# Kernel optimization log

Hardware: AMD Instinct MI355X
Metric: run time of the kernel (lower is better)

Reference implementation:

```python
import jax, jax.numpy as jnp
import numpy as np

TEMPERATURE = 0.01  # clamped min is 0.01, so constant temp stays 0.01
MASK_VAL = -10000.0


def setup_inputs() -> dict:
    key = jax.random.key(0)
    k1, k2 = jax.random.split(key)
    B, C, D = 512, 16, 128
    ts_features = jax.random.normal(k1, (B, C, D), dtype=jnp.float32)
    note_features = jax.random.normal(k2, (B, C, D), dtype=jnp.float32)
    return {"ts_features": ts_features, "note_features": note_features}


def reference(ts_features, note_features):
    B, C, D = ts_features.shape
    N = B * C
    ts = ts_features.reshape(N, D)
    nt = note_features.reshape(N, D)

    # sim[i, j] = <ts_i, nt_j>
    sim = jnp.einsum('id,jd->ij', ts, nt)

    # block-diagonal mask: within each CxC block, off-diagonal -> -10000, diagonal kept
    idx = jnp.arange(N)
    blk = idx // C
    same_block = blk[:, None] == blk[None, :]
    is_diag = idx[:, None] == idx[None, :]
    sim_new = jnp.where(same_block & ~is_diag, jnp.asarray(MASK_VAL, sim.dtype), sim)

    logits = sim_new / TEMPERATURE
    # cross entropy with labels = arange(N), both directions
    lsm_r = jax.nn.log_softmax(logits, axis=-1)
    lsm_c = jax.nn.log_softmax(logits.T, axis=-1)
    diag_ids = (idx, idx)
    ce_r = -jnp.mean(lsm_r[diag_ids])
    ce_c = -jnp.mean(lsm_c[diag_ids])
    total_loss = (ce_r + ce_c) / 2

    # nan/inf -> 0 as in the original
    total_loss = jnp.where(jnp.isnan(total_loss) | jnp.isinf(total_loss),
                           jnp.asarray(0.0, total_loss.dtype), total_loss)
    return total_loss
```

## Files before the change

kernel.cpp:

```cpp
#include <hip/hip_runtime.h>
#include <stdint.h>

#define NROWS 8192
#define DDIM  128
#define PPART 8
#define BROWS 256
#define NITER 16
#define LOG2E_X100 144.26950408889634f
#define LN2F       0.6931471805599453f

typedef __bf16 bf16x8 __attribute__((ext_vector_type(8)));
typedef float  f32x4  __attribute__((ext_vector_type(4)));
typedef unsigned short u16x8 __attribute__((ext_vector_type(8)));


__device__ __forceinline__ unsigned short f2bf_rne(float f) {
    union { float f; uint32_t u; } v; v.f = f;
    uint32_t r = (v.u + 0x7FFFu + ((v.u >> 16) & 1u)) >> 16;
    return (unsigned short)r;
}

__device__ __forceinline__ void async16(const unsigned short* g, unsigned char* l) {
    __builtin_amdgcn_global_load_lds(
        (const __attribute__((address_space(1))) unsigned int*)g,
        (__attribute__((address_space(3))) unsigned int*)l, 16, 0, 0);
}

__global__ void convert_kernel(const float* __restrict__ ts, const float* __restrict__ nt,
                               unsigned short* __restrict__ ts_bf,
                               unsigned short* __restrict__ nt_bf,
                               float* __restrict__ acc, int* __restrict__ ticket) {
    const int nchunk = (NROWS * DDIM) / 8;
    int tid = blockIdx.x * blockDim.x + threadIdx.x;
    bool isNT = tid >= nchunk;
    int i = isNT ? (tid - nchunk) : tid;
    const float4* src = (const float4*)(isNT ? nt : ts) + i * 2;
    float4 v0 = src[0], v1 = src[1];
    float sc = isNT ? 1.0f : LOG2E_X100;
    u16x8 o;
    o[0] = f2bf_rne(v0.x * sc); o[1] = f2bf_rne(v0.y * sc);
    o[2] = f2bf_rne(v0.z * sc); o[3] = f2bf_rne(v0.w * sc);
    o[4] = f2bf_rne(v1.x * sc); o[5] = f2bf_rne(v1.y * sc);
    o[6] = f2bf_rne(v1.z * sc); o[7] = f2bf_rne(v1.w * sc);
    int row = i >> 4, chunk = i & 15;
    int g = row >> 4, c = row & 15;
    int kc = chunk >> 2, quad = chunk & 3;
    int off16 = (g * 4 + kc) * 64 + quad * 16 + c;
    ((u16x8*)(isNT ? nt_bf : ts_bf))[off16] = o;
    if (tid == 0) { *acc = 0.0f; *ticket = 0; }
}

__device__ __forceinline__ void dma_stage(const unsigned short* g, unsigned char* l,
                                          int lane, int wv) {
#pragma unroll
    for (int k = 0; k < 2; ++k) {
        int u = wv * 2 + k;
        async16(g + u * 512 + lane * 8, l + u * 1024);
    }
}

__global__ __launch_bounds__(512, 4) void rowstats_kernel(
        const unsigned short* __restrict__ ts_bf,
        const unsigned short* __restrict__ nt_bf,
        float* __restrict__ pm, float* __restrict__ ps, float* __restrict__ pd) {
    __shared__ unsigned char smem[2 * 16384];

    const int lane = threadIdx.x & 63;
    const int wv   = threadIdx.x >> 6;
    const int c    = lane & 15;
    const int quad = lane >> 4;
    const int bx   = blockIdx.x;
    const int part = blockIdx.y;
    const int dir  = blockIdx.z;
    const int rows0 = bx * BROWS + wv * 32;

    const unsigned short* A = dir ? nt_bf : ts_bf;
    const unsigned short* B = dir ? ts_bf : nt_bf;

    const int G0 = bx * 16 + wv * 2;
    bf16x8 a[2][4];
#pragma unroll
    for (int s = 0; s < 2; ++s)
#pragma unroll
        for (int kc = 0; kc < 4; ++kc)
            a[s][kc] = *(const bf16x8*)(A + ((G0 + s) * 4 + kc) * 512 + lane * 8);

    float m[2][4], ss[2][4], dg[2][4];
#pragma unroll
    for (int s = 0; s < 2; ++s)
#pragma unroll
        for (int r = 0; r < 4; ++r) { m[s][r] = -INFINITY; ss[s][r] = 0.0f; dg[s][r] = 0.0f; }

    const bool havePart = (part == (bx >> 2));
    const int  t_d = (bx & 3) * 4 + (wv >> 1);
    const int  l0  = (wv & 1) * 2;

    const unsigned short* bwalk = B + part * 64 * 2048;

    dma_stage(bwalk, smem, lane, wv);
    __syncthreads();

    for (int t = 0; t < NITER; ++t) {
        if (t + 1 < NITER)
            dma_stage(bwalk + (t + 1) * 8192, smem + ((t + 1) & 1) * 16384, lane, wv);

        const unsigned char* buf = smem + (t & 1) * 16384 + lane * 16;

        f32x4 av[4][2];
#pragma unroll
        for (int l = 0; l < 4; ++l)
#pragma unroll
            for (int s = 0; s < 2; ++s) av[l][s] = (f32x4){0.f, 0.f, 0.f, 0.f};

#pragma unroll
        for (int kc = 0; kc < 4; ++kc) {
            bf16x8 b0 = *(const bf16x8*)(buf + kc * 1024);
            bf16x8 b1 = *(const bf16x8*)(buf + kc * 1024 + 4096);
            bf16x8 b2 = *(const bf16x8*)(buf + kc * 1024 + 8192);
            bf16x8 b3 = *(const bf16x8*)(buf + kc * 1024 + 12288);
            av[0][0] = __builtin_amdgcn_mfma_f32_16x16x32_bf16(a[0][kc], b0, av[0][0], 0, 0, 0);
            av[0][1] = __builtin_amdgcn_mfma_f32_16x16x32_bf16(a[1][kc], b0, av[0][1], 0, 0, 0);
            av[1][0] = __builtin_amdgcn_mfma_f32_16x16x32_bf16(a[0][kc], b1, av[1][0], 0, 0, 0);
            av[1][1] = __builtin_amdgcn_mfma_f32_16x16x32_bf16(a[1][kc], b1, av[1][1], 0, 0, 0);
            av[2][0] = __builtin_amdgcn_mfma_f32_16x16x32_bf16(a[0][kc], b2, av[2][0], 0, 0, 0);
            av[2][1] = __builtin_amdgcn_mfma_f32_16x16x32_bf16(a[1][kc], b2, av[2][1], 0, 0, 0);
            av[3][0] = __builtin_amdgcn_mfma_f32_16x16x32_bf16(a[0][kc], b3, av[3][0], 0, 0, 0);
            av[3][1] = __builtin_amdgcn_mfma_f32_16x16x32_bf16(a[1][kc], b3, av[3][1], 0, 0, 0);
        }

        const bool pd_ = havePart && (t == t_d);
#pragma unroll
        for (int s = 0; s < 2; ++s) {
#pragma unroll
            for (int r = 0; r < 4; ++r) {
                float x0 = av[0][s][r], x1 = av[1][s][r];
                float x2 = av[2][s][r], x3 = av[3][s][r];
                if (pd_) {
                    const int dslot = l0 + s;
                    bool onDiag = (c == quad * 4 + r);
                    float xv = dslot == 0 ? x0 : dslot == 1 ? x1 : dslot == 2 ? x2 : x3;
                    if (onDiag) dg[s][r] += xv;
                    float rep = onDiag ? xv : -1.0e30f;
                    if (dslot == 0) x0 = rep; else if (dslot == 1) x1 = rep;
                    else if (dslot == 2) x2 = rep; else x3 = rep;
                }
                float mn = fmaxf(fmaxf(fmaxf(x0, x1), fmaxf(x2, x3)), m[s][r]);
                float e  = __builtin_amdgcn_exp2f(m[s][r] - mn);
                float es = (__builtin_amdgcn_exp2f(x0 - mn) + __builtin_amdgcn_exp2f(x1 - mn))
                         + (__builtin_amdgcn_exp2f(x2 - mn) + __builtin_amdgcn_exp2f(x3 - mn));
                ss[s][r] = fmaf(ss[s][r], e, es);
                m[s][r] = mn;
            }
        }
        __syncthreads();
    }

#pragma unroll
    for (int s = 0; s < 2; ++s) {
#pragma unroll
        for (int r = 0; r < 4; ++r) {
            float mm = m[s][r];
#pragma unroll
            for (int off = 1; off < 16; off <<= 1)
                mm = fmaxf(mm, __shfl_xor(mm, off, 64));
            float sv = ss[s][r] * __builtin_amdgcn_exp2f(m[s][r] - mm);
            float dd = dg[s][r];
#pragma unroll
            for (int off = 1; off < 16; off <<= 1) {
                sv += __shfl_xor(sv, off, 64);
                dd += __shfl_xor(dd, off, 64);
            }
            if (c == 0) {
                int row = rows0 + s * 16 + quad * 4 + r;
                int idx = (dir * NROWS + row) * PPART + part;
                pm[idx] = mm; ps[idx] = sv; pd[idx] = dd;
            }
        }
    }
}

__global__ void merge_kernel(const float* __restrict__ pm, const float* __restrict__ ps,
                             const float* __restrict__ pd, float* __restrict__ acc,
                             int* __restrict__ ticket, float* __restrict__ out) {
    int tid = blockIdx.x * blockDim.x + threadIdx.x;
    const float* pmr = pm + tid * PPART;
    const float* psr = ps + tid * PPART;
    const float* pdr = pd + tid * PPART;
    float mt = -INFINITY;
#pragma unroll
    for (int p = 0; p < PPART; ++p) mt = fmaxf(mt, pmr[p]);
    float st = 0.0f, dt = 0.0f;
#pragma unroll
    for (int p = 0; p < PPART; ++p) {
        st += psr[p] * __builtin_amdgcn_exp2f(pmr[p] - mt);
        dt += pdr[p];
    }
    float lsm = dt - mt - __builtin_amdgcn_logf(st);

    float v = lsm;
#pragma unroll
    for (int off = 32; off; off >>= 1) v += __shfl_down(v, off, 64);
    __shared__ float wsum[4];
    if ((threadIdx.x & 63) == 0) wsum[threadIdx.x >> 6] = v;
    __syncthreads();
    if (threadIdx.x == 0) {
        atomicAdd(acc, wsum[0] + wsum[1] + wsum[2] + wsum[3]);
        __threadfence();
        int old = atomicAdd(ticket, 1);
        if (old == (int)gridDim.x - 1) {
            __threadfence();
            float tot = atomicAdd(acc, 0.0f);
            float t = -(tot * LN2F) / (2.0f * NROWS);
            if (!isfinite(t)) t = 0.0f;
            out[0] = t;
        }
    }
}

extern "C" void kernel_launch(void* const* d_in, const int* in_sizes, int n_in,
                              void* d_out, int out_size, void* d_ws, size_t ws_size,
                              hipStream_t stream) {
    const float* ts = (const float*)d_in[0];
    const float* nt = (const float*)d_in[1];
    float* out = (float*)d_out;

    unsigned short* ts_bf = (unsigned short*)d_ws;
    unsigned short* nt_bf = ts_bf + NROWS * DDIM;
    float* pm = (float*)(nt_bf + NROWS * DDIM);
    float* ps = pm + 2 * NROWS * PPART;
    float* pd = ps + 2 * NROWS * PPART;
    float* acc = pd + 2 * NROWS * PPART;
    int* ticket = (int*)(acc + 1);

    convert_kernel<<<1024, 256, 0, stream>>>(ts, nt, ts_bf, nt_bf, acc, ticket);
    rowstats_kernel<<<dim3(NROWS / BROWS, PPART, 2), 512, 0, stream>>>(ts_bf, nt_bf, pm, ps, pd);
    merge_kernel<<<(2 * NROWS) / 256, 256, 0, stream>>>(pm, ps, pd, acc, ticket, out);
}
```

Before: 107.4 us.

## Compute row and column softmax stats from one shared similarity tile

Each 256x256 block of the similarity matrix is now computed once, and both its row-wise and column-wise log-sum-exp partials are reduced from it. Previously the matrix was computed twice, once per direction. This halves the MFMA work. In exchange the kernel does extra exp2 and cross-lane shuffles for the column reduction, adds LDS traffic, and the merge kernel reads 32 partials per row for each of rows and columns.

```diff
diff --git a/kernel.cpp b/kernel.cpp
--- a/kernel.cpp
+++ b/kernel.cpp
@@ -3,9 +3,7 @@
 
 #define NROWS 8192
 #define DDIM  128
-#define PPART 8
-#define BROWS 256
-#define NITER 16
+#define NBLK  32
 #define LOG2E_X100 144.26950408889634f
 #define LN2F       0.6931471805599453f
 
@@ -59,31 +57,29 @@
     }
 }
 
-__global__ __launch_bounds__(512, 4) void rowstats_kernel(
+__global__ __launch_bounds__(512, 4) void tile_kernel(
         const unsigned short* __restrict__ ts_bf,
         const unsigned short* __restrict__ nt_bf,
-        float* __restrict__ pm, float* __restrict__ ps, float* __restrict__ pd) {
+        float* __restrict__ pm, float* __restrict__ ps, float* __restrict__ pd,
+        float* __restrict__ cm, float* __restrict__ cs) {
     __shared__ unsigned char smem[2 * 16384];
+    __shared__ float2 colp[8][256];
 
     const int lane = threadIdx.x & 63;
     const int wv   = threadIdx.x >> 6;
     const int c    = lane & 15;
     const int quad = lane >> 4;
-    const int bx   = blockIdx.x;
-    const int part = blockIdx.y;
-    const int dir  = blockIdx.z;
-    const int rows0 = bx * BROWS + wv * 32;
-
-    const unsigned short* A = dir ? nt_bf : ts_bf;
-    const unsigned short* B = dir ? ts_bf : nt_bf;
-
-    const int G0 = bx * 16 + wv * 2;
+    const int I    = blockIdx.x;
+    const int J    = blockIdx.y;
+    const int rows0 = I * 256 + wv * 32;
+
+    const int G0 = I * 16 + wv * 2;
     bf16x8 a[2][4];
 #pragma unroll
     for (int s = 0; s < 2; ++s)
 #pragma unroll
         for (int kc = 0; kc < 4; ++kc)
-            a[s][kc] = *(const bf16x8*)(A + ((G0 + s) * 4 + kc) * 512 + lane * 8);
+            a[s][kc] = *(const bf16x8*)(ts_bf + ((G0 + s) * 4 + kc) * 512 + lane * 8);
 
     float m[2][4], ss[2][4], dg[2][4];
 #pragma unroll
@@ -91,17 +87,17 @@
 #pragma unroll
         for (int r = 0; r < 4; ++r) { m[s][r] = -INFINITY; ss[s][r] = 0.0f; dg[s][r] = 0.0f; }
 
-    const bool havePart = (part == (bx >> 2));
-    const int  t_d = (bx & 3) * 4 + (wv >> 1);
+    const bool diagB = (I == J);
+    const int  t_d = wv >> 1;
     const int  l0  = (wv & 1) * 2;
 
-    const unsigned short* bwalk = B + part * 64 * 2048;
+    const unsigned short* bwalk = nt_bf + J * 16 * 2048;
 
     dma_stage(bwalk, smem, lane, wv);
     __syncthreads();
 
-    for (int t = 0; t < NITER; ++t) {
-        if (t + 1 < NITER)
+    for (int t = 0; t < 4; ++t) {
+        if (t + 1 < 4)
             dma_stage(bwalk + (t + 1) * 8192, smem + ((t + 1) & 1) * 16384, lane, wv);
 
         const unsigned char* buf = smem + (t & 1) * 16384 + lane * 16;
@@ -128,7 +124,7 @@
             av[3][1] = __builtin_amdgcn_mfma_f32_16x16x32_bf16(a[1][kc], b3, av[3][1], 0, 0, 0);
         }
 
-        const bool pd_ = havePart && (t == t_d);
+        const bool pd_ = diagB && (t == t_d);
 #pragma unroll
         for (int s = 0; s < 2; ++s) {
 #pragma unroll
@@ -143,6 +139,8 @@
                     float rep = onDiag ? xv : -1.0e30f;
                     if (dslot == 0) x0 = rep; else if (dslot == 1) x1 = rep;
                     else if (dslot == 2) x2 = rep; else x3 = rep;
+                    av[0][s][r] = x0; av[1][s][r] = x1;
+                    av[2][s][r] = x2; av[3][s][r] = x3;
                 }
                 float mn = fmaxf(fmaxf(fmaxf(x0, x1), fmaxf(x2, x3)), m[s][r]);
                 float e  = __builtin_amdgcn_exp2f(m[s][r] - mn);
@@ -152,6 +150,27 @@
                 m[s][r] = mn;
             }
         }
+
+#pragma unroll
+        for (int l = 0; l < 4; ++l) {
+            float v0 = av[l][0][0], v1 = av[l][0][1], v2 = av[l][0][2], v3 = av[l][0][3];
+            float w0 = av[l][1][0], w1 = av[l][1][1], w2 = av[l][1][2], w3 = av[l][1][3];
+            float m8 = fmaxf(fmaxf(fmaxf(v0, v1), fmaxf(v2, v3)),
+                             fmaxf(fmaxf(w0, w1), fmaxf(w2, w3)));
+            float s8 = ((__builtin_amdgcn_exp2f(v0 - m8) + __builtin_amdgcn_exp2f(v1 - m8))
+                      + (__builtin_amdgcn_exp2f(v2 - m8) + __builtin_amdgcn_exp2f(v3 - m8)))
+                     + ((__builtin_amdgcn_exp2f(w0 - m8) + __builtin_amdgcn_exp2f(w1 - m8))
+                      + (__builtin_amdgcn_exp2f(w2 - m8) + __builtin_amdgcn_exp2f(w3 - m8)));
+#pragma unroll
+            for (int off = 16; off < 64; off <<= 1) {
+                float m2 = __shfl_xor(m8, off, 64);
+                float s2 = __shfl_xor(s8, off, 64);
+                float mn = fmaxf(m8, m2);
+                s8 = s8 * __builtin_amdgcn_exp2f(m8 - mn) + s2 * __builtin_amdgcn_exp2f(m2 - mn);
+                m8 = mn;
+            }
+            if (quad == 0) colp[wv][t * 64 + l * 16 + c] = make_float2(m8, s8);
+        }
         __syncthreads();
     }
 
@@ -172,32 +191,52 @@
             }
             if (c == 0) {
                 int row = rows0 + s * 16 + quad * 4 + r;
-                int idx = (dir * NROWS + row) * PPART + part;
+                int idx = row * NBLK + J;
                 pm[idx] = mm; ps[idx] = sv; pd[idx] = dd;
             }
         }
     }
+
+    __syncthreads();
+    int j = threadIdx.x;
+    if (j < 256) {
+        float2 p = colp[0][j];
+        float M = p.x, S = p.y;
+#pragma unroll
+        for (int w = 1; w < 8; ++w) {
+            float2 q = colp[w][j];
+            float mn = fmaxf(M, q.x);
+            S = S * __builtin_amdgcn_exp2f(M - mn) + q.y * __builtin_amdgcn_exp2f(q.x - mn);
+            M = mn;
+        }
+        int col = J * 256 + j;
+        cm[col * NBLK + I] = M;
+        cs[col * NBLK + I] = S;
+    }
 }
 
 __global__ void merge_kernel(const float* __restrict__ pm, const float* __restrict__ ps,
-                             const float* __restrict__ pd, float* __restrict__ acc,
+                             const float* __restrict__ pd, const float* __restrict__ cm,
+                             const float* __restrict__ cs, float* __restrict__ acc,
                              int* __restrict__ ticket, float* __restrict__ out) {
-    int tid = blockIdx.x * blockDim.x + threadIdx.x;
-    const float* pmr = pm + tid * PPART;
-    const float* psr = ps + tid * PPART;
-    const float* pdr = pd + tid * PPART;
-    float mt = -INFINITY;
-#pragma unroll
-    for (int p = 0; p < PPART; ++p) mt = fmaxf(mt, pmr[p]);
-    float st = 0.0f, dt = 0.0f;
-#pragma unroll
-    for (int p = 0; p < PPART; ++p) {
+    int i = blockIdx.x * blockDim.x + threadIdx.x;
+    const float* pmr = pm + i * NBLK;
+    const float* psr = ps + i * NBLK;
+    const float* pdr = pd + i * NBLK;
+    const float* cmr = cm + i * NBLK;
+    const float* csr = cs + i * NBLK;
+    float mt = -INFINITY, mc = -INFINITY;
+#pragma unroll
+    for (int p = 0; p < NBLK; ++p) { mt = fmaxf(mt, pmr[p]); mc = fmaxf(mc, cmr[p]); }
+    float st = 0.0f, sc = 0.0f, dt = 0.0f;
+#pragma unroll
+    for (int p = 0; p < NBLK; ++p) {
         st += psr[p] * __builtin_amdgcn_exp2f(pmr[p] - mt);
+        sc += csr[p] * __builtin_amdgcn_exp2f(cmr[p] - mc);
         dt += pdr[p];
     }
-    float lsm = dt - mt - __builtin_amdgcn_logf(st);
-
-    float v = lsm;
+    float v = 2.0f * dt - mt - __builtin_amdgcn_logf(st)
+                      - mc - __builtin_amdgcn_logf(sc);
 #pragma unroll
     for (int off = 32; off; off >>= 1) v += __shfl_down(v, off, 64);
     __shared__ float wsum[4];
@@ -227,12 +266,14 @@
     unsigned short* ts_bf = (unsigned short*)d_ws;
     unsigned short* nt_bf = ts_bf + NROWS * DDIM;
     float* pm = (float*)(nt_bf + NROWS * DDIM);
-    float* ps = pm + 2 * NROWS * PPART;
-    float* pd = ps + 2 * NROWS * PPART;
-    float* acc = pd + 2 * NROWS * PPART;
+    float* ps = pm + NROWS * NBLK;
+    float* pd = ps + NROWS * NBLK;
+    float* cm = pd + NROWS * NBLK;
+    float* cs = cm + NROWS * NBLK;
+    float* acc = cs + NROWS * NBLK;
     int* ticket = (int*)(acc + 1);
 
     convert_kernel<<<1024, 256, 0, stream>>>(ts, nt, ts_bf, nt_bf, acc, ticket);
-    rowstats_kernel<<<dim3(NROWS / BROWS, PPART, 2), 512, 0, stream>>>(ts_bf, nt_bf, pm, ps, pd);
-    merge_kernel<<<(2 * NROWS) / 256, 256, 0, stream>>>(pm, ps, pd, acc, ticket, out);
-}
+    tile_kernel<<<dim3(NBLK, NBLK), 512, 0, stream>>>(ts_bf, nt_bf, pm, ps, pd, cm, cs);
+    merge_kernel<<<NROWS / 256, 256, 0, stream>>>(pm, ps, pd, cm, cs, acc, ticket, out);
+}
```

New measurement: 181.6 us. +69.1%, slower.
